# Kernel tuning notes

Measured on AMD Instinct MI355X. Metric: run time of the kernel, lower is better.

The kernel has to match this reference:

```python
import jax, jax.numpy as jnp
import numpy as np

BETA = 0.25
CODEBOOK_SIZE = 8192
EMB_DIM = 256


def setup_inputs() -> dict:
    key = jax.random.key(0)
    k1, k2 = jax.random.split(key)
    z_e = jax.random.normal(k1, (32, 32, 32, EMB_DIM), dtype=jnp.float32)
    codebook = jax.random.normal(k2, (CODEBOOK_SIZE, EMB_DIM), dtype=jnp.float32) * 0.05
    return {"z_e": z_e, "codebook": codebook}


def reference(z_e, codebook):
    sg = jax.lax.stop_gradient
    D = codebook.shape[1]
    z = z_e.reshape(-1, D)                                   # [N, D]
    # squared euclidean distances via ||z||^2 + ||e||^2 - 2 z.e
    z_sq = jnp.sum(z * z, axis=1, keepdims=True)             # [N, 1]
    e_sq = jnp.sum(codebook * codebook, axis=1)              # [K]
    distances = z_sq + e_sq[None, :] - 2.0 * (z @ codebook.T)  # [N, K]
    indices = jnp.argmin(distances, axis=1)                  # [N]
    z_q = codebook[indices].reshape(z_e.shape)               # gather

    commitment = jnp.mean((sg(z_e) - z_q) ** 2)
    codebook_loss = jnp.mean((z_e - sg(z_q)) ** 2)
    z_q_st = z_e + sg(z_q - z_e)
    loss_vq = codebook_loss + BETA * commitment

    # perplexity of assignment distribution (no grad)
    N = z.shape[0]
    counts = jnp.zeros((codebook.shape[0],), jnp.float32).at[indices].add(1.0)
    avg_probs = counts / N
    perplexity = jnp.exp(-jnp.sum(avg_probs * jnp.log(avg_probs + 1e-12)))

    return z_q_st, indices.reshape(z_e.shape[:-1]), loss_vq, perplexity
```

## Files before the change

kernel.cpp:

```cpp
#include <hip/hip_runtime.h>
#include <math.h>

#define N_TOT 32768
#define K_CB 8192
#define D_DIM 256

#define OUT_IDX  (N_TOT * D_DIM)
#define OUT_LOSS (OUT_IDX + N_TOT)
#define OUT_PERP (OUT_LOSS + 1)

#define WS_AIMG   0u
#define AIMG_SZ   (256u * 16u * 8192u)
#define WS_BIMG   (WS_AIMG + AIMG_SZ)
#define BIMG_SZ   (64u * 16u * 8192u)
#define WS_PART   (WS_BIMG + BIMG_SZ)
#define PART_SZ   (16u * 32768u * 16u)
#define WS_ESQ    (WS_PART + PART_SZ)
#define WS_COUNTS (WS_ESQ + 32768u)
#define WS_LPART  (WS_COUNTS + 32768u)

typedef short bf16x8 __attribute__((ext_vector_type(8)));
typedef float f32x4  __attribute__((ext_vector_type(4)));
typedef unsigned short u16x8 __attribute__((ext_vector_type(8)));

__device__ __forceinline__ unsigned short f2bf(float x) {
  unsigned int b = __float_as_uint(x);
  b = b + 0x7FFFu + ((b >> 16) & 1u);
  return (unsigned short)(b >> 16);
}
__device__ __forceinline__ float bf2f(unsigned short h) {
  return __uint_as_float(((unsigned int)h) << 16);
}
__device__ __forceinline__ void gld16(const void* g, void* l) {
  __builtin_amdgcn_global_load_lds(
      (const __attribute__((address_space(1))) void*)g,
      (__attribute__((address_space(3))) void*)l, 16, 0, 0);
}

__global__ __launch_bounds__(256) void prep_z(const float* __restrict__ Z,
                                              char* __restrict__ Aimg) {
  const int tid = threadIdx.x;
  const int row = blockIdx.x * 8 + (tid >> 5);
  const int ch = tid & 31;
  const int kt = ch >> 2, c = ch & 3;
  const int rb = row >> 7, r = row & 127;
  const float4 z0 = *(const float4*)(Z + (size_t)row * D_DIM + kt * 32 + c * 8);
  const float4 z1 = *(const float4*)(Z + (size_t)row * D_DIM + kt * 32 + c * 8 + 4);
  u16x8 h, l;
  h[0] = f2bf(z0.x); l[0] = f2bf(z0.x - bf2f(h[0]));
  h[1] = f2bf(z0.y); l[1] = f2bf(z0.y - bf2f(h[1]));
  h[2] = f2bf(z0.z); l[2] = f2bf(z0.z - bf2f(h[2]));
  h[3] = f2bf(z0.w); l[3] = f2bf(z0.w - bf2f(h[3]));
  h[4] = f2bf(z1.x); l[4] = f2bf(z1.x - bf2f(h[4]));
  h[5] = f2bf(z1.y); l[5] = f2bf(z1.y - bf2f(h[5]));
  h[6] = f2bf(z1.z); l[6] = f2bf(z1.z - bf2f(h[6]));
  h[7] = f2bf(z1.w); l[7] = f2bf(z1.w - bf2f(h[7]));
  const int cs = c ^ ((r >> 1) & 3);
  const size_t off = (size_t)r * 64 + cs * 16;
  *(u16x8*)(Aimg + (size_t)(rb * 16 + kt) * 8192 + off) = h;
  *(u16x8*)(Aimg + (size_t)(rb * 16 + 8 + kt) * 8192 + off) = l;
}

__global__ __launch_bounds__(256) void prep_e(const float* __restrict__ E,
                                              char* __restrict__ Bimg,
                                              float* __restrict__ esqg) {
  const int tid = threadIdx.x;
  const int code = blockIdx.x * 8 + (tid >> 5);
  const int ch = tid & 31;
  const int kt = ch >> 2, c = ch & 3;
  const int ntg = code >> 7, r = code & 127;
  const float4 e0 = *(const float4*)(E + (size_t)code * D_DIM + kt * 32 + c * 8);
  const float4 e1 = *(const float4*)(E + (size_t)code * D_DIM + kt * 32 + c * 8 + 4);
  u16x8 h, l;
  h[0] = f2bf(e0.x); l[0] = f2bf(e0.x - bf2f(h[0]));
  h[1] = f2bf(e0.y); l[1] = f2bf(e0.y - bf2f(h[1]));
  h[2] = f2bf(e0.z); l[2] = f2bf(e0.z - bf2f(h[2]));
  h[3] = f2bf(e0.w); l[3] = f2bf(e0.w - bf2f(h[3]));
  h[4] = f2bf(e1.x); l[4] = f2bf(e1.x - bf2f(h[4]));
  h[5] = f2bf(e1.y); l[5] = f2bf(e1.y - bf2f(h[5]));
  h[6] = f2bf(e1.z); l[6] = f2bf(e1.z - bf2f(h[6]));
  h[7] = f2bf(e1.w); l[7] = f2bf(e1.w - bf2f(h[7]));
  const int cs = c ^ ((r >> 1) & 3);
  const size_t off = (size_t)r * 64 + cs * 16;
  *(u16x8*)(Bimg + (size_t)(ntg * 16 + kt) * 8192 + off) = h;
  *(u16x8*)(Bimg + (size_t)(ntg * 16 + 8 + kt) * 8192 + off) = l;
  float s = e0.x * e0.x + e0.y * e0.y + e0.z * e0.z + e0.w * e0.w +
            e1.x * e1.x + e1.y * e1.y + e1.z * e1.z + e1.w * e1.w;
#pragma unroll
  for (int o = 16; o > 0; o >>= 1) s += __shfl_down(s, o, 32);
  if ((tid & 31) == 0) esqg[code] = s;
}

__global__ __launch_bounds__(256, 2) void argmin_mfma(
    const char* __restrict__ Aimg, const char* __restrict__ Bimg,
    const float* __restrict__ esqg, float4* __restrict__ partials) {
  __shared__ __align__(16) union {
    struct { char Ah[8192]; char Al[8192]; char Bh[8192]; char Bl[8192]; } t[2];
    float4 mbuf[128][2];
  } u;
  __shared__ float esq_s[512];

  const int tid = threadIdx.x;
  const int lane = tid & 63;
  const int wid = tid >> 6;
  const int wrow = wid >> 1, wcol = wid & 1;
  const int lrow = lane & 15, lgrp = lane >> 4;
  const int cb = blockIdx.x & 7;
  const int ntp = (blockIdx.x >> 3) & 1;
  const int rb = blockIdx.x >> 4;
  const int ntg0 = cb * 8 + ntp * 4;

  const int sw = (lrow >> 1) & 3;
  const int aoff = (wrow * 64 + lrow) * 64 + (lgrp ^ sw) * 16;
  const int boff = (wcol * 64 + lrow) * 64 + (lgrp ^ sw) * 16;
  const char* Abase = Aimg + (size_t)rb * (16u * 8192u);
  const char* Bbase0 = Bimg + (size_t)ntg0 * (16u * 8192u);
  const int soff = tid * 16;

  float s1[16], s2[16]; int c1[16], c2[16];
#pragma unroll
  for (int i = 0; i < 16; i++) { s1[i] = 3.4e38f; s2[i] = 3.4e38f; c1[i] = 0; c2[i] = 0; }

#define STAGE_K(kk, BI) do {                                                   \
    const int k_ = (kk) & 7, nti_ = (kk) >> 3;                                 \
    const char* ah_ = Abase + (size_t)k_ * 8192;                               \
    const char* al_ = Abase + (size_t)(8 + k_) * 8192;                         \
    const char* bb_ = Bbase0 + (size_t)nti_ * (16u * 8192u);                   \
    const char* bh_ = bb_ + (size_t)k_ * 8192;                                 \
    const char* bl_ = bb_ + (size_t)(8 + k_) * 8192;                           \
    gld16(ah_ + soff,        u.t[BI].Ah + soff);                               \
    gld16(ah_ + 4096 + soff, u.t[BI].Ah + 4096 + soff);                        \
    gld16(al_ + soff,        u.t[BI].Al + soff);                               \
    gld16(al_ + 4096 + soff, u.t[BI].Al + 4096 + soff);                        \
    gld16(bh_ + soff,        u.t[BI].Bh + soff);                               \
    gld16(bh_ + 4096 + soff, u.t[BI].Bh + 4096 + soff);                        \
    gld16(bl_ + soff,        u.t[BI].Bl + soff);                               \
    gld16(bl_ + 4096 + soff, u.t[BI].Bl + 4096 + soff);                        \
  } while (0)

#define COMPUTE_K(BI) do {                                                     \
    bf16x8 afh[4], afl[4], bfh[4], bfl[4];                                     \
    _Pragma("unroll")                                                          \
    for (int rf = 0; rf < 4; rf++) {                                           \
      afh[rf] = *(const bf16x8*)(u.t[BI].Ah + aoff + rf * 1024);               \
      afl[rf] = *(const bf16x8*)(u.t[BI].Al + aoff + rf * 1024);               \
    }                                                                          \
    _Pragma("unroll")                                                          \
    for (int cf = 0; cf < 4; cf++) {                                           \
      bfh[cf] = *(const bf16x8*)(u.t[BI].Bh + boff + cf * 1024);               \
      bfl[cf] = *(const bf16x8*)(u.t[BI].Bl + boff + cf * 1024);               \
    }                                                                          \
    _Pragma("unroll")                                                          \
    for (int rf = 0; rf < 4; rf++)                                             \
      _Pragma("unroll")                                                        \
      for (int cf = 0; cf < 4; cf++) {                                         \
        acc[rf][cf] = __builtin_amdgcn_mfma_f32_16x16x32_bf16(afh[rf], bfh[cf], acc[rf][cf], 0, 0, 0); \
        acc[rf][cf] = __builtin_amdgcn_mfma_f32_16x16x32_bf16(afh[rf], bfl[cf], acc[rf][cf], 0, 0, 0); \
        acc[rf][cf] = __builtin_amdgcn_mfma_f32_16x16x32_bf16(afl[rf], bfh[cf], acc[rf][cf], 0, 0, 0); \
      }                                                                        \
  } while (0)

  esq_s[tid] = esqg[ntg0 * 128 + tid];
  esq_s[tid + 256] = esqg[ntg0 * 128 + tid + 256];
  STAGE_K(0, 0);

  f32x4 acc[4][4];
#pragma unroll
  for (int i = 0; i < 4; i++)
#pragma unroll
    for (int j = 0; j < 4; j++) acc[i][j] = (f32x4){0.f, 0.f, 0.f, 0.f};

  __syncthreads();

  for (int kp = 0; kp < 16; kp++) {
    const int kk0 = kp * 2;
    STAGE_K(kk0 + 1, 1);
    COMPUTE_K(0);
    __syncthreads();
    if (kp < 15) STAGE_K(kk0 + 2, 0);
    COMPUTE_K(1);
    if ((kp & 3) == 3) {
      const int nti = kp >> 2;
      const int ntg = ntg0 + nti;
      const int code0 = ntg * 128 + wcol * 64 + lrow;
      float eq[4];
#pragma unroll
      for (int cf = 0; cf < 4; cf++) eq[cf] = esq_s[nti * 128 + wcol * 64 + cf * 16 + lrow];
#pragma unroll
      for (int rf = 0; rf < 4; rf++)
#pragma unroll
        for (int reg = 0; reg < 4; reg++) {
          const int r = rf * 4 + reg;
          float v0 = fmaf(-2.f, acc[rf][0][reg], eq[0]);
          float v1 = fmaf(-2.f, acc[rf][1][reg], eq[1]);
          float v2 = fmaf(-2.f, acc[rf][2][reg], eq[2]);
          float v3 = fmaf(-2.f, acc[rf][3][reg], eq[3]);
          float a1 = v0, a2 = v1; int ka1 = code0, ka2 = code0 + 16;
          if (v1 < v0) { a1 = v1; ka1 = code0 + 16; a2 = v0; ka2 = code0; }
          float b1v = v2, b2v = v3; int kb1 = code0 + 32, kb2 = code0 + 48;
          if (v3 < v2) { b1v = v3; kb1 = code0 + 48; b2v = v2; kb2 = code0 + 32; }
          float m1, m2; int k1, k2;
          if (a1 <= b1v) {
            m1 = a1; k1 = ka1;
            if (b1v < a2) { m2 = b1v; k2 = kb1; } else { m2 = a2; k2 = ka2; }
          } else {
            m1 = b1v; k1 = kb1;
            if (a1 <= b2v) { m2 = a1; k2 = ka1; } else { m2 = b2v; k2 = kb2; }
          }
          if (m1 < s1[r]) {
            s2[r] = (m2 < s1[r]) ? m2 : s1[r];
            c2[r] = (m2 < s1[r]) ? k2 : c1[r];
            s1[r] = m1; c1[r] = k1;
          } else if (m1 < s2[r]) {
            s2[r] = m1; c2[r] = k1;
          }
        }
#pragma unroll
      for (int i = 0; i < 4; i++)
#pragma unroll
        for (int j = 0; j < 4; j++) acc[i][j] = (f32x4){0.f, 0.f, 0.f, 0.f};
    }
    __syncthreads();
  }
#undef STAGE_K
#undef COMPUTE_K

#pragma unroll
  for (int r = 0; r < 16; r++) {
#pragma unroll
    for (int m = 1; m <= 8; m <<= 1) {
      float o1 = __shfl_xor(s1[r], m); int k1 = __shfl_xor(c1[r], m);
      float o2 = __shfl_xor(s2[r], m); int k2 = __shfl_xor(c2[r], m);
      bool t1 = (o1 < s1[r]) || (o1 == s1[r] && k1 < c1[r]);
      bool t2 = (o1 < s2[r]) || (o1 == s2[r] && k1 < c2[r]);
      float ns2 = t1 ? s1[r] : (t2 ? o1 : s2[r]);
      int   nc2 = t1 ? c1[r] : (t2 ? k1 : c2[r]);
      s1[r] = t1 ? o1 : s1[r]; c1[r] = t1 ? k1 : c1[r];
      s2[r] = ns2; c2[r] = nc2;
      bool u1 = (o2 < s1[r]) || (o2 == s1[r] && k2 < c1[r]);
      bool u2 = (o2 < s2[r]) || (o2 == s2[r] && k2 < c2[r]);
      ns2 = u1 ? s1[r] : (u2 ? o2 : s2[r]);
      nc2 = u1 ? c1[r] : (u2 ? k2 : c2[r]);
      s1[r] = u1 ? o2 : s1[r]; c1[r] = u1 ? k2 : c1[r];
      s2[r] = ns2; c2[r] = nc2;
    }
  }

  __syncthreads();
  if (lrow == 0) {
#pragma unroll
    for (int rf = 0; rf < 4; rf++)
#pragma unroll
      for (int reg = 0; reg < 4; reg++) {
        const int r = rf * 4 + reg;
        const int row = wrow * 64 + rf * 16 + lgrp * 4 + reg;
        float4 p;
        p.x = s1[r]; p.y = __int_as_float(c1[r]);
        p.z = s2[r]; p.w = __int_as_float(c2[r]);
        u.mbuf[row][wcol] = p;
      }
  }
  __syncthreads();
  if (tid < 128) {
    float4 pa = u.mbuf[tid][0];
    float4 pb = u.mbuf[tid][1];
    float D1 = pa.x; int C1 = __float_as_int(pa.y);
    float D2 = pa.z; int C2 = __float_as_int(pa.w);
    float a = pb.x; int ka = __float_as_int(pb.y);
    float b = pb.z; int kb = __float_as_int(pb.w);
    if (a < D1 || (a == D1 && ka < C1)) { D2 = D1; C2 = C1; D1 = a; C1 = ka; }
    else if (a < D2 || (a == D2 && ka < C2)) { D2 = a; C2 = ka; }
    if (b < D1 || (b == D1 && kb < C1)) { D2 = D1; C2 = C1; D1 = b; C1 = kb; }
    else if (b < D2 || (b == D2 && kb < C2)) { D2 = b; C2 = kb; }
    float4 p;
    p.x = D1; p.y = __int_as_float(C1); p.z = D2; p.w = __int_as_float(C2);
    partials[(size_t)(ntp * 8 + cb) * N_TOT + rb * 128 + tid] = p;
  }
}

__global__ __launch_bounds__(128) void merge_rescore(
    const float* __restrict__ Z, const float* __restrict__ E,
    const float4* __restrict__ partials, float* __restrict__ out_idx_f) {
  const int row = blockIdx.x * 128 + threadIdx.x;
  float D1 = 3.4e38f, D2 = 3.4e38f; int C1 = 0, C2 = 0;
  for (int s = 0; s < 16; s++) {
    float4 p = partials[(size_t)s * N_TOT + row];
    float a = p.x; int ka = __float_as_int(p.y);
    float b = p.z; int kb = __float_as_int(p.w);
    if (a < D1 || (a == D1 && ka < C1)) { D2 = D1; C2 = C1; D1 = a; C1 = ka; }
    else if (a < D2 || (a == D2 && ka < C2)) { D2 = a; C2 = ka; }
    if (b < D1 || (b == D1 && kb < C1)) { D2 = D1; C2 = C1; D1 = b; C1 = kb; }
    else if (b < D2 || (b == D2 && kb < C2)) { D2 = b; C2 = kb; }
  }
  const float* zp = Z + (size_t)row * D_DIM;
  const float* ep1 = E + (size_t)C1 * D_DIM;
  const float* ep2 = E + (size_t)C2 * D_DIM;
  double dd1 = 0.0, dd2 = 0.0;
  for (int d = 0; d < D_DIM; d += 4) {
    const float4 zv = *(const float4*)(zp + d);
    const float4 e1v = *(const float4*)(ep1 + d);
    const float4 e2v = *(const float4*)(ep2 + d);
    double t;
    t = (double)zv.x - (double)e1v.x; dd1 += t * t;
    t = (double)zv.y - (double)e1v.y; dd1 += t * t;
    t = (double)zv.z - (double)e1v.z; dd1 += t * t;
    t = (double)zv.w - (double)e1v.w; dd1 += t * t;
    t = (double)zv.x - (double)e2v.x; dd2 += t * t;
    t = (double)zv.y - (double)e2v.y; dd2 += t * t;
    t = (double)zv.z - (double)e2v.z; dd2 += t * t;
    t = (double)zv.w - (double)e2v.w; dd2 += t * t;
  }
  int fin = C1;
  if (dd2 < dd1 || (dd2 == dd1 && C2 < C1)) fin = C2;
  out_idx_f[row] = (float)fin;
}

__global__ __launch_bounds__(256) void gather_kernel(
    const float* __restrict__ Z, const float* __restrict__ E,
    const float* __restrict__ idx_f, float* __restrict__ zq_out,
    float* __restrict__ counts, float* __restrict__ loss_part) {
  const int t = threadIdx.x;
  float lsum = 0.0f;
  for (int rr = 0; rr < 16; rr++) {
    const int row = blockIdx.x * 16 + rr;
    const int c = (int)idx_f[row];
    const float e = E[(size_t)c * D_DIM + t];
    const float z = Z[(size_t)row * D_DIM + t];
    zq_out[(size_t)row * D_DIM + t] = e;
    const float d = z - e;
    lsum += d * d;
    if (t == 0) atomicAdd(&counts[c], 1.0f);
  }
#pragma unroll
  for (int off = 32; off > 0; off >>= 1) lsum += __shfl_down(lsum, off);
  __shared__ float wsum[4];
  if ((t & 63) == 0) wsum[t >> 6] = lsum;
  __syncthreads();
  if (t == 0) loss_part[blockIdx.x] = wsum[0] + wsum[1] + wsum[2] + wsum[3];
}

__global__ __launch_bounds__(256) void final_kernel(
    const float* __restrict__ counts, const float* __restrict__ loss_part,
    float* __restrict__ out) {
  const int t = threadIdx.x;
  float h = 0.0f, ls = 0.0f;
  for (int k = t; k < K_CB; k += 256) {
    const float p = counts[k] * (1.0f / (float)N_TOT);
    h += p * logf(p + 1e-12f);
  }
  for (int k = t; k < 2048; k += 256) ls += loss_part[k];
#pragma unroll
  for (int off = 32; off > 0; off >>= 1) {
    h += __shfl_down(h, off);
    ls += __shfl_down(ls, off);
  }
  __shared__ float ws4[4], ls4[4];
  if ((t & 63) == 0) { ws4[t >> 6] = h; ls4[t >> 6] = ls; }
  __syncthreads();
  if (t == 0) {
    const float H = ws4[0] + ws4[1] + ws4[2] + ws4[3];
    const float L = ls4[0] + ls4[1] + ls4[2] + ls4[3];
    out[OUT_LOSS] = 1.25f * L * (1.0f / (float)(N_TOT * D_DIM));
    out[OUT_PERP] = expf(-H);
  }
}

extern "C" void kernel_launch(void* const* d_in, const int* in_sizes, int n_in,
                              void* d_out, int out_size, void* d_ws, size_t ws_size,
                              hipStream_t stream) {
  (void)in_sizes; (void)n_in; (void)out_size; (void)ws_size;
  const float* Z = (const float*)d_in[0];
  const float* E = (const float*)d_in[1];
  float* out = (float*)d_out;
  char* ws = (char*)d_ws;
  char* Aimg = ws + WS_AIMG;
  char* Bimg = ws + WS_BIMG;
  float4* partials = (float4*)(ws + WS_PART);
  float* esqg = (float*)(ws + WS_ESQ);
  float* counts = (float*)(ws + WS_COUNTS);
  float* loss_part = (float*)(ws + WS_LPART);

  hipMemsetAsync(ws + WS_COUNTS, 0, 32768, stream);
  prep_z<<<dim3(4096), dim3(256), 0, stream>>>(Z, Aimg);
  prep_e<<<dim3(1024), dim3(256), 0, stream>>>(E, Bimg, esqg);
  argmin_mfma<<<dim3(4096), dim3(256), 0, stream>>>(Aimg, Bimg, esqg, partials);
  merge_rescore<<<dim3(256), dim3(128), 0, stream>>>(Z, E, partials, out + OUT_IDX);
  gather_kernel<<<dim3(2048), dim3(256), 0, stream>>>(Z, E, out + OUT_IDX, out, counts, loss_part);
  final_kernel<<<dim3(1), dim3(256), 0, stream>>>(counts, loss_part, out);
}
```

Baseline: 666.8 us.

## Enlarge argmin MFMA tile to 256x256 with 8 waves and s_setprio scheduling

The distance GEMM kernel moves from 128x128 tiles with 4 waves to 256x256 tiles with 8 waves per block, 512 codes per block and half as many blocks. This raises arithmetic intensity and cuts redundant global loads of the A and B images. The main loop now uses explicit barriers with vmcnt waits and s_setprio around the MFMA groups to overlap staging with compute. Running top-2 state moves from registers into an LDS merge buffer per epilogue. The change doubles LDS use to about 128KB and doubles accumulator registers, which risks lower occupancy or spills.

```diff
diff --git a/kernel.cpp b/kernel.cpp
--- a/kernel.cpp
+++ b/kernel.cpp
@@ -91,190 +91,199 @@
   if ((tid & 31) == 0) esqg[code] = s;
 }
 
-__global__ __launch_bounds__(256, 2) void argmin_mfma(
+__global__ __launch_bounds__(512, 2) void argmin_mfma(
     const char* __restrict__ Aimg, const char* __restrict__ Bimg,
     const float* __restrict__ esqg, float4* __restrict__ partials) {
-  __shared__ __align__(16) union {
-    struct { char Ah[8192]; char Al[8192]; char Bh[8192]; char Bl[8192]; } t[2];
-    float4 mbuf[128][2];
-  } u;
+  __shared__ __align__(16) struct { char Ah[16384]; char Al[16384];
+                                    char Bh[16384]; char Bl[16384]; } lds[2];
+  __shared__ __align__(16) float4 mrg[256][4];
   __shared__ float esq_s[512];
 
   const int tid = threadIdx.x;
   const int lane = tid & 63;
   const int wid = tid >> 6;
-  const int wrow = wid >> 1, wcol = wid & 1;
+  const int wrow = wid >> 2, wcol = wid & 3;
   const int lrow = lane & 15, lgrp = lane >> 4;
-  const int cb = blockIdx.x & 7;
-  const int ntp = (blockIdx.x >> 3) & 1;
   const int rb = blockIdx.x >> 4;
-  const int ntg0 = cb * 8 + ntp * 4;
+  const int ct = blockIdx.x & 15;
+  const int rb2 = rb * 2;
+  const int so = tid * 16;
 
   const int sw = (lrow >> 1) & 3;
-  const int aoff = (wrow * 64 + lrow) * 64 + (lgrp ^ sw) * 16;
-  const int boff = (wcol * 64 + lrow) * 64 + (lgrp ^ sw) * 16;
-  const char* Abase = Aimg + (size_t)rb * (16u * 8192u);
-  const char* Bbase0 = Bimg + (size_t)ntg0 * (16u * 8192u);
-  const int soff = tid * 16;
-
-  float s1[16], s2[16]; int c1[16], c2[16];
-#pragma unroll
-  for (int i = 0; i < 16; i++) { s1[i] = 3.4e38f; s2[i] = 3.4e38f; c1[i] = 0; c2[i] = 0; }
-
-#define STAGE_K(kk, BI) do {                                                   \
-    const int k_ = (kk) & 7, nti_ = (kk) >> 3;                                 \
-    const char* ah_ = Abase + (size_t)k_ * 8192;                               \
-    const char* al_ = Abase + (size_t)(8 + k_) * 8192;                         \
-    const char* bb_ = Bbase0 + (size_t)nti_ * (16u * 8192u);                   \
-    const char* bh_ = bb_ + (size_t)k_ * 8192;                                 \
-    const char* bl_ = bb_ + (size_t)(8 + k_) * 8192;                           \
-    gld16(ah_ + soff,        u.t[BI].Ah + soff);                               \
-    gld16(ah_ + 4096 + soff, u.t[BI].Ah + 4096 + soff);                        \
-    gld16(al_ + soff,        u.t[BI].Al + soff);                               \
-    gld16(al_ + 4096 + soff, u.t[BI].Al + 4096 + soff);                        \
-    gld16(bh_ + soff,        u.t[BI].Bh + soff);                               \
-    gld16(bh_ + 4096 + soff, u.t[BI].Bh + 4096 + soff);                        \
-    gld16(bl_ + soff,        u.t[BI].Bl + soff);                               \
-    gld16(bl_ + 4096 + soff, u.t[BI].Bl + 4096 + soff);                        \
+  const int slot = (lgrp ^ sw) * 16;
+  const int abase = wrow * 8192 + lrow * 64 + slot;
+  const int bbase = (wcol >> 1) * 8192 + ((wcol & 1) * 64 + lrow) * 64 + slot;
+
+#define STAGE_K(cn, BI) do {                                                   \
+    const int k_ = (cn) & 7, t_ = (cn) >> 3;                                   \
+    const int ga_ = rb2 * 16 + k_, gb_ = (rb2 + 1) * 16 + k_;                  \
+    const int g0_ = (ct * 4 + t_ * 2) * 16 + k_, g1_ = g0_ + 16;               \
+    gld16(Aimg + (size_t)ga_ * 8192 + so,       lds[BI].Ah + so);              \
+    gld16(Aimg + (size_t)gb_ * 8192 + so,       lds[BI].Ah + 8192 + so);       \
+    gld16(Aimg + (size_t)(ga_ + 8) * 8192 + so, lds[BI].Al + so);              \
+    gld16(Aimg + (size_t)(gb_ + 8) * 8192 + so, lds[BI].Al + 8192 + so);       \
+    gld16(Bimg + (size_t)g0_ * 8192 + so,       lds[BI].Bh + so);              \
+    gld16(Bimg + (size_t)g1_ * 8192 + so,       lds[BI].Bh + 8192 + so);       \
+    gld16(Bimg + (size_t)(g0_ + 8) * 8192 + so, lds[BI].Bl + so);              \
+    gld16(Bimg + (size_t)(g1_ + 8) * 8192 + so, lds[BI].Bl + 8192 + so);       \
   } while (0)
 
 #define COMPUTE_K(BI) do {                                                     \
-    bf16x8 afh[4], afl[4], bfh[4], bfl[4];                                     \
-    _Pragma("unroll")                                                          \
-    for (int rf = 0; rf < 4; rf++) {                                           \
-      afh[rf] = *(const bf16x8*)(u.t[BI].Ah + aoff + rf * 1024);               \
-      afl[rf] = *(const bf16x8*)(u.t[BI].Al + aoff + rf * 1024);               \
+    bf16x8 fa[8], fb[4], fc[4];                                                \
+    _Pragma("unroll")                                                          \
+    for (int rf = 0; rf < 8; rf++)                                             \
+      fa[rf] = *(const bf16x8*)(lds[BI].Ah + abase + rf * 1024);               \
+    _Pragma("unroll")                                                          \
+    for (int cf = 0; cf < 4; cf++)                                             \
+      fb[cf] = *(const bf16x8*)(lds[BI].Bh + bbase + cf * 1024);               \
+    __builtin_amdgcn_s_setprio(1);                                             \
+    _Pragma("unroll")                                                          \
+    for (int rf = 0; rf < 8; rf++)                                             \
+      _Pragma("unroll")                                                        \
+      for (int cf = 0; cf < 4; cf++)                                           \
+        acc[rf][cf] = __builtin_amdgcn_mfma_f32_16x16x32_bf16(fa[rf], fb[cf], acc[rf][cf], 0, 0, 0); \
+    __builtin_amdgcn_s_setprio(0);                                             \
+    _Pragma("unroll")                                                          \
+    for (int cf = 0; cf < 4; cf++)                                             \
+      fc[cf] = *(const bf16x8*)(lds[BI].Bl + bbase + cf * 1024);               \
+    __builtin_amdgcn_s_setprio(1);                                             \
+    _Pragma("unroll")                                                          \
+    for (int rf = 0; rf < 8; rf++)                                             \
+      _Pragma("unroll")                                                        \
+      for (int cf = 0; cf < 4; cf++)                                           \
+        acc[rf][cf] = __builtin_amdgcn_mfma_f32_16x16x32_bf16(fa[rf], fc[cf], acc[rf][cf], 0, 0, 0); \
+    __builtin_amdgcn_s_setprio(0);                                             \
+    _Pragma("unroll")                                                          \
+    for (int rf = 0; rf < 8; rf++)                                             \
+      fa[rf] = *(const bf16x8*)(lds[BI].Al + abase + rf * 1024);               \
+    __builtin_amdgcn_s_setprio(1);                                             \
+    _Pragma("unroll")                                                          \
+    for (int rf = 0; rf < 8; rf++)                                             \
+      _Pragma("unroll")                                                        \
+      for (int cf = 0; cf < 4; cf++)                                           \
+        acc[rf][cf] = __builtin_amdgcn_mfma_f32_16x16x32_bf16(fa[rf], fb[cf], acc[rf][cf], 0, 0, 0); \
+    __builtin_amdgcn_s_setprio(0);                                             \
+  } while (0)
+
+#define CHUNK(c_, BI, DOSTAGE) do {                                            \
+    __builtin_amdgcn_sched_barrier(0);                                         \
+    __builtin_amdgcn_s_barrier();                                              \
+    if (DOSTAGE) { STAGE_K((c_) + 1, (BI) ^ 1);                                \
+                   asm volatile("s_waitcnt vmcnt(8)" ::: "memory"); }          \
+    else         { asm volatile("s_waitcnt vmcnt(0)" ::: "memory"); }          \
+    __builtin_amdgcn_s_barrier();                                              \
+    __builtin_amdgcn_sched_barrier(0);                                         \
+    COMPUTE_K(BI);                                                             \
+  } while (0)
+
+#define EPILOGUE(T) do {                                                       \
+    const float eqA = esq_s[(T) * 256 + wcol * 64 + lrow];                     \
+    const float eqB = esq_s[(T) * 256 + wcol * 64 + 16 + lrow];                \
+    const float eqC = esq_s[(T) * 256 + wcol * 64 + 32 + lrow];                \
+    const float eqD = esq_s[(T) * 256 + wcol * 64 + 48 + lrow];                \
+    const int code0 = ct * 512 + (T) * 256 + wcol * 64 + lrow;                 \
+    _Pragma("unroll")                                                          \
+    for (int rf = 0; rf < 8; rf++)                                             \
+      _Pragma("unroll")                                                        \
+      for (int reg = 0; reg < 4; reg++) {                                      \
+        float v0 = fmaf(-2.f, acc[rf][0][reg], eqA);                           \
+        float v1 = fmaf(-2.f, acc[rf][1][reg], eqB);                           \
+        float v2 = fmaf(-2.f, acc[rf][2][reg], eqC);                           \
+        float v3 = fmaf(-2.f, acc[rf][3][reg], eqD);                           \
+        float a1 = v0, a2 = v1; int ka1 = code0, ka2 = code0 + 16;             \
+        if (v1 < v0) { a1 = v1; ka1 = code0 + 16; a2 = v0; ka2 = code0; }      \
+        float b1 = v2, b2 = v3; int kb1 = code0 + 32, kb2 = code0 + 48;        \
+        if (v3 < v2) { b1 = v3; kb1 = code0 + 48; b2 = v2; kb2 = code0 + 32; } \
+        float m1, m2; int k1, k2;                                              \
+        if (a1 <= b1) { m1 = a1; k1 = ka1;                                     \
+          if (b1 < a2) { m2 = b1; k2 = kb1; } else { m2 = a2; k2 = ka2; } }    \
+        else { m1 = b1; k1 = kb1;                                              \
+          if (a1 <= b2) { m2 = a1; k2 = ka1; } else { m2 = b2; k2 = kb2; } }   \
+        _Pragma("unroll")                                                      \
+        for (int mm = 1; mm <= 8; mm <<= 1) {                                  \
+          float o1 = __shfl_xor(m1, mm); int j1 = __shfl_xor(k1, mm);          \
+          float o2 = __shfl_xor(m2, mm); int j2 = __shfl_xor(k2, mm);          \
+          bool t1 = (o1 < m1) || (o1 == m1 && j1 < k1);                        \
+          bool t2 = (o1 < m2) || (o1 == m2 && j1 < k2);                        \
+          float ns2 = t1 ? m1 : (t2 ? o1 : m2);                                \
+          int   nc2 = t1 ? k1 : (t2 ? j1 : k2);                                \
+          m1 = t1 ? o1 : m1; k1 = t1 ? j1 : k1; m2 = ns2; k2 = nc2;            \
+          bool u1 = (o2 < m1) || (o2 == m1 && j2 < k1);                        \
+          bool u2 = (o2 < m2) || (o2 == m2 && j2 < k2);                        \
+          ns2 = u1 ? m1 : (u2 ? o2 : m2);                                      \
+          nc2 = u1 ? k1 : (u2 ? j2 : k2);                                      \
+          m1 = u1 ? o2 : m1; k1 = u1 ? j2 : k1; m2 = ns2; k2 = nc2;            \
+        }                                                                      \
+        if (lrow == 0) {                                                       \
+          const int row = wrow * 128 + rf * 16 + lgrp * 4 + reg;               \
+          if ((T) == 0) {                                                      \
+            float4 p; p.x = m1; p.y = __int_as_float(k1);                      \
+            p.z = m2; p.w = __int_as_float(k2);                                \
+            mrg[row][wcol] = p;                                                \
+          } else {                                                             \
+            float4 p = mrg[row][wcol];                                         \
+            float D1 = p.x; int C1 = __float_as_int(p.y);                      \
+            float D2 = p.z; int C2 = __float_as_int(p.w);                      \
+            if (m1 < D1 || (m1 == D1 && k1 < C1)) { D2 = D1; C2 = C1; D1 = m1; C1 = k1; } \
+            else if (m1 < D2 || (m1 == D2 && k1 < C2)) { D2 = m1; C2 = k1; }   \
+            if (m2 < D1 || (m2 == D1 && k2 < C1)) { D2 = D1; C2 = C1; D1 = m2; C1 = k2; } \
+            else if (m2 < D2 || (m2 == D2 && k2 < C2)) { D2 = m2; C2 = k2; }   \
+            p.x = D1; p.y = __int_as_float(C1);                                \
+            p.z = D2; p.w = __int_as_float(C2);                                \
+            mrg[row][wcol] = p;                                                \
+          }                                                                    \
+        }                                                                      \
+      }                                                                        \
+    if ((T) == 0) {                                                            \
+      _Pragma("unroll")                                                        \
+      for (int i = 0; i < 8; i++)                                              \
+        _Pragma("unroll")                                                      \
+        for (int j = 0; j < 4; j++) acc[i][j] = (f32x4){0.f, 0.f, 0.f, 0.f};   \
     }                                                                          \
-    _Pragma("unroll")                                                          \
-    for (int cf = 0; cf < 4; cf++) {                                           \
-      bfh[cf] = *(const bf16x8*)(u.t[BI].Bh + boff + cf * 1024);               \
-      bfl[cf] = *(const bf16x8*)(u.t[BI].Bl + boff + cf * 1024);               \
-    }                                                                          \
-    _Pragma("unroll")                                                          \
-    for (int rf = 0; rf < 4; rf++)                                             \
-      _Pragma("unroll")                                                        \
-      for (int cf = 0; cf < 4; cf++) {                                         \
-        acc[rf][cf] = __builtin_amdgcn_mfma_f32_16x16x32_bf16(afh[rf], bfh[cf], acc[rf][cf], 0, 0, 0); \
-        acc[rf][cf] = __builtin_amdgcn_mfma_f32_16x16x32_bf16(afh[rf], bfl[cf], acc[rf][cf], 0, 0, 0); \
-        acc[rf][cf] = __builtin_amdgcn_mfma_f32_16x16x32_bf16(afl[rf], bfh[cf], acc[rf][cf], 0, 0, 0); \
-      }                                                                        \
   } while (0)
 
-  esq_s[tid] = esqg[ntg0 * 128 + tid];
-  esq_s[tid + 256] = esqg[ntg0 * 128 + tid + 256];
+  f32x4 acc[8][4];
+#pragma unroll
+  for (int i = 0; i < 8; i++)
+#pragma unroll
+    for (int j = 0; j < 4; j++) acc[i][j] = (f32x4){0.f, 0.f, 0.f, 0.f};
+
+  esq_s[tid] = esqg[ct * 512 + tid];
   STAGE_K(0, 0);
-
-  f32x4 acc[4][4];
-#pragma unroll
-  for (int i = 0; i < 4; i++)
-#pragma unroll
-    for (int j = 0; j < 4; j++) acc[i][j] = (f32x4){0.f, 0.f, 0.f, 0.f};
-
   __syncthreads();
 
-  for (int kp = 0; kp < 16; kp++) {
-    const int kk0 = kp * 2;
-    STAGE_K(kk0 + 1, 1);
-    COMPUTE_K(0);
-    __syncthreads();
-    if (kp < 15) STAGE_K(kk0 + 2, 0);
-    COMPUTE_K(1);
-    if ((kp & 3) == 3) {
-      const int nti = kp >> 2;
-      const int ntg = ntg0 + nti;
-      const int code0 = ntg * 128 + wcol * 64 + lrow;
-      float eq[4];
-#pragma unroll
-      for (int cf = 0; cf < 4; cf++) eq[cf] = esq_s[nti * 128 + wcol * 64 + cf * 16 + lrow];
-#pragma unroll
-      for (int rf = 0; rf < 4; rf++)
-#pragma unroll
-        for (int reg = 0; reg < 4; reg++) {
-          const int r = rf * 4 + reg;
-          float v0 = fmaf(-2.f, acc[rf][0][reg], eq[0]);
-          float v1 = fmaf(-2.f, acc[rf][1][reg], eq[1]);
-          float v2 = fmaf(-2.f, acc[rf][2][reg], eq[2]);
-          float v3 = fmaf(-2.f, acc[rf][3][reg], eq[3]);
-          float a1 = v0, a2 = v1; int ka1 = code0, ka2 = code0 + 16;
-          if (v1 < v0) { a1 = v1; ka1 = code0 + 16; a2 = v0; ka2 = code0; }
-          float b1v = v2, b2v = v3; int kb1 = code0 + 32, kb2 = code0 + 48;
-          if (v3 < v2) { b1v = v3; kb1 = code0 + 48; b2v = v2; kb2 = code0 + 32; }
-          float m1, m2; int k1, k2;
-          if (a1 <= b1v) {
-            m1 = a1; k1 = ka1;
-            if (b1v < a2) { m2 = b1v; k2 = kb1; } else { m2 = a2; k2 = ka2; }
-          } else {
-            m1 = b1v; k1 = kb1;
-            if (a1 <= b2v) { m2 = a1; k2 = ka1; } else { m2 = b2v; k2 = kb2; }
-          }
-          if (m1 < s1[r]) {
-            s2[r] = (m2 < s1[r]) ? m2 : s1[r];
-            c2[r] = (m2 < s1[r]) ? k2 : c1[r];
-            s1[r] = m1; c1[r] = k1;
-          } else if (m1 < s2[r]) {
-            s2[r] = m1; c2[r] = k1;
-          }
-        }
-#pragma unroll
-      for (int i = 0; i < 4; i++)
-#pragma unroll
-        for (int j = 0; j < 4; j++) acc[i][j] = (f32x4){0.f, 0.f, 0.f, 0.f};
-    }
-    __syncthreads();
-  }
+  for (int c2 = 0; c2 < 8; c2++) {
+    const int c0 = c2 * 2;
+    CHUNK(c0, 0, 1);
+    if (c2 < 7) CHUNK(c0 + 1, 1, 1);
+    else        CHUNK(15, 1, 0);
+    if (c2 == 3) EPILOGUE(0);
+  }
+  EPILOGUE(1);
+
 #undef STAGE_K
 #undef COMPUTE_K
-
-#pragma unroll
-  for (int r = 0; r < 16; r++) {
-#pragma unroll
-    for (int m = 1; m <= 8; m <<= 1) {
-      float o1 = __shfl_xor(s1[r], m); int k1 = __shfl_xor(c1[r], m);
-      float o2 = __shfl_xor(s2[r], m); int k2 = __shfl_xor(c2[r], m);
-      bool t1 = (o1 < s1[r]) || (o1 == s1[r] && k1 < c1[r]);
-      bool t2 = (o1 < s2[r]) || (o1 == s2[r] && k1 < c2[r]);
-      float ns2 = t1 ? s1[r] : (t2 ? o1 : s2[r]);
-      int   nc2 = t1 ? c1[r] : (t2 ? k1 : c2[r]);
-      s1[r] = t1 ? o1 : s1[r]; c1[r] = t1 ? k1 : c1[r];
-      s2[r] = ns2; c2[r] = nc2;
-      bool u1 = (o2 < s1[r]) || (o2 == s1[r] && k2 < c1[r]);
-      bool u2 = (o2 < s2[r]) || (o2 == s2[r] && k2 < c2[r]);
-      ns2 = u1 ? s1[r] : (u2 ? o2 : s2[r]);
-      nc2 = u1 ? c1[r] : (u2 ? k2 : c2[r]);
-      s1[r] = u1 ? o2 : s1[r]; c1[r] = u1 ? k2 : c1[r];
-      s2[r] = ns2; c2[r] = nc2;
+#undef CHUNK
+#undef EPILOGUE
+
+  __syncthreads();
+  if (tid < 256) {
+    float4 q = mrg[tid][0];
+    float D1 = q.x; int C1 = __float_as_int(q.y);
+    float D2 = q.z; int C2 = __float_as_int(q.w);
+#pragma unroll
+    for (int w = 1; w < 4; w++) {
+      float4 p = mrg[tid][w];
+      float a = p.x; int ka = __float_as_int(p.y);
+      float b = p.z; int kb = __float_as_int(p.w);
+      if (a < D1 || (a == D1 && ka < C1)) { D2 = D1; C2 = C1; D1 = a; C1 = ka; }
+      else if (a < D2 || (a == D2 && ka < C2)) { D2 = a; C2 = ka; }
+      if (b < D1 || (b == D1 && kb < C1)) { D2 = D1; C2 = C1; D1 = b; C1 = kb; }
+      else if (b < D2 || (b == D2 && kb < C2)) { D2 = b; C2 = kb; }
     }
-  }
-
-  __syncthreads();
-  if (lrow == 0) {
-#pragma unroll
-    for (int rf = 0; rf < 4; rf++)
-#pragma unroll
-      for (int reg = 0; reg < 4; reg++) {
-        const int r = rf * 4 + reg;
-        const int row = wrow * 64 + rf * 16 + lgrp * 4 + reg;
-        float4 p;
-        p.x = s1[r]; p.y = __int_as_float(c1[r]);
-        p.z = s2[r]; p.w = __int_as_float(c2[r]);
-        u.mbuf[row][wcol] = p;
-      }
-  }
-  __syncthreads();
-  if (tid < 128) {
-    float4 pa = u.mbuf[tid][0];
-    float4 pb = u.mbuf[tid][1];
-    float D1 = pa.x; int C1 = __float_as_int(pa.y);
-    float D2 = pa.z; int C2 = __float_as_int(pa.w);
-    float a = pb.x; int ka = __float_as_int(pb.y);
-    float b = pb.z; int kb = __float_as_int(pb.w);
-    if (a < D1 || (a == D1 && ka < C1)) { D2 = D1; C2 = C1; D1 = a; C1 = ka; }
-    else if (a < D2 || (a == D2 && ka < C2)) { D2 = a; C2 = ka; }
-    if (b < D1 || (b == D1 && kb < C1)) { D2 = D1; C2 = C1; D1 = b; C1 = kb; }
-    else if (b < D2 || (b == D2 && kb < C2)) { D2 = b; C2 = kb; }
     float4 p;
     p.x = D1; p.y = __int_as_float(C1); p.z = D2; p.w = __int_as_float(C2);
-    partials[(size_t)(ntp * 8 + cb) * N_TOT + rb * 128 + tid] = p;
+    partials[(size_t)ct * N_TOT + rb * 256 + tid] = p;
   }
 }
 
@@ -383,7 +392,7 @@
   hipMemsetAsync(ws + WS_COUNTS, 0, 32768, stream);
   prep_z<<<dim3(4096), dim3(256), 0, stream>>>(Z, Aimg);
   prep_e<<<dim3(1024), dim3(256), 0, stream>>>(E, Bimg, esqg);
-  argmin_mfma<<<dim3(4096), dim3(256), 0, stream>>>(Aimg, Bimg, esqg, partials);
+  argmin_mfma<<<dim3(2048), dim3(512), 0, stream>>>(Aimg, Bimg, esqg, partials);
   merge_rescore<<<dim3(256), dim3(128), 0, stream>>>(Z, E, partials, out + OUT_IDX);
   gather_kernel<<<dim3(2048), dim3(256), 0, stream>>>(Z, E, out + OUT_IDX, out, counts, loss_part);
   final_kernel<<<dim3(1), dim3(256), 0, stream>>>(counts, loss_part, out);
```

After: 1.876 ms. 2.81x slower.

## Restructure GEMM main loop with explicit vmcnt waits, barriers and MFMA priority

Applied to the files above, without the earlier changes.

Replaces the two-stage-per-iteration loop with a fully unrolled 32-step loop that issues the next K-slice's async global-to-LDS loads and then waits only on the older loads via an explicit s_waitcnt vmcnt(8), surrounded by raw s_barrier and sched_barrier fences. The MFMA block is split into three phases (hi*hi, hi*lo, lo*hi), each wrapped in s_setprio to favour the matrix work, and the argmin epilogue is moved into a macro called every 8 steps. The goal is to overlap loads with MFMA and cut synchronisation stalls. The cost is hand-tuned wait counts that depend on how many loads STAGE_K issues, plus larger code from full unrolling.

```diff
diff --git a/kernel.cpp b/kernel.cpp
--- a/kernel.cpp
+++ b/kernel.cpp
@@ -150,14 +150,65 @@
       bfh[cf] = *(const bf16x8*)(u.t[BI].Bh + boff + cf * 1024);               \
       bfl[cf] = *(const bf16x8*)(u.t[BI].Bl + boff + cf * 1024);               \
     }                                                                          \
+    __builtin_amdgcn_s_setprio(1);                                             \
     _Pragma("unroll")                                                          \
     for (int rf = 0; rf < 4; rf++)                                             \
       _Pragma("unroll")                                                        \
-      for (int cf = 0; cf < 4; cf++) {                                         \
+      for (int cf = 0; cf < 4; cf++)                                           \
         acc[rf][cf] = __builtin_amdgcn_mfma_f32_16x16x32_bf16(afh[rf], bfh[cf], acc[rf][cf], 0, 0, 0); \
+    __builtin_amdgcn_s_setprio(0);                                             \
+    __builtin_amdgcn_s_setprio(1);                                             \
+    _Pragma("unroll")                                                          \
+    for (int rf = 0; rf < 4; rf++)                                             \
+      _Pragma("unroll")                                                        \
+      for (int cf = 0; cf < 4; cf++)                                           \
         acc[rf][cf] = __builtin_amdgcn_mfma_f32_16x16x32_bf16(afh[rf], bfl[cf], acc[rf][cf], 0, 0, 0); \
+    __builtin_amdgcn_s_setprio(0);                                             \
+    __builtin_amdgcn_s_setprio(1);                                             \
+    _Pragma("unroll")                                                          \
+    for (int rf = 0; rf < 4; rf++)                                             \
+      _Pragma("unroll")                                                        \
+      for (int cf = 0; cf < 4; cf++)                                           \
         acc[rf][cf] = __builtin_amdgcn_mfma_f32_16x16x32_bf16(afl[rf], bfh[cf], acc[rf][cf], 0, 0, 0); \
+    __builtin_amdgcn_s_setprio(0);                                             \
+  } while (0)
+
+#define EPILOGUE(T) do {                                                       \
+    const int code0 = (ntg0 + (T)) * 128 + wcol * 64 + lrow;                   \
+    float eq0 = esq_s[(T) * 128 + wcol * 64 + lrow];                           \
+    float eq1 = esq_s[(T) * 128 + wcol * 64 + 16 + lrow];                      \
+    float eq2 = esq_s[(T) * 128 + wcol * 64 + 32 + lrow];                      \
+    float eq3 = esq_s[(T) * 128 + wcol * 64 + 48 + lrow];                      \
+    _Pragma("unroll")                                                          \
+    for (int rf = 0; rf < 4; rf++)                                             \
+      _Pragma("unroll")                                                        \
+      for (int reg = 0; reg < 4; reg++) {                                      \
+        const int r = rf * 4 + reg;                                            \
+        float v0 = fmaf(-2.f, acc[rf][0][reg], eq0);                           \
+        float v1 = fmaf(-2.f, acc[rf][1][reg], eq1);                           \
+        float v2 = fmaf(-2.f, acc[rf][2][reg], eq2);                           \
+        float v3 = fmaf(-2.f, acc[rf][3][reg], eq3);                           \
+        float a1 = v0, a2 = v1; int ka1 = code0, ka2 = code0 + 16;             \
+        if (v1 < v0) { a1 = v1; ka1 = code0 + 16; a2 = v0; ka2 = code0; }      \
+        float b1v = v2, b2v = v3; int kb1 = code0 + 32, kb2 = code0 + 48;      \
+        if (v3 < v2) { b1v = v3; kb1 = code0 + 48; b2v = v2; kb2 = code0 + 32; } \
+        float m1, m2; int k1, k2;                                              \
+        if (a1 <= b1v) { m1 = a1; k1 = ka1;                                    \
+          if (b1v < a2) { m2 = b1v; k2 = kb1; } else { m2 = a2; k2 = ka2; } }  \
+        else { m1 = b1v; k1 = kb1;                                             \
+          if (a1 <= b2v) { m2 = a1; k2 = ka1; } else { m2 = b2v; k2 = kb2; } } \
+        if (m1 < s1[r]) {                                                      \
+          s2[r] = (m2 < s1[r]) ? m2 : s1[r];                                   \
+          c2[r] = (m2 < s1[r]) ? k2 : c1[r];                                   \
+          s1[r] = m1; c1[r] = k1;                                              \
+        } else if (m1 < s2[r]) {                                               \
+          s2[r] = m1; c2[r] = k1;                                              \
+        }                                                                      \
       }                                                                        \
+    _Pragma("unroll")                                                          \
+    for (int i = 0; i < 4; i++)                                                \
+      _Pragma("unroll")                                                        \
+      for (int j = 0; j < 4; j++) acc[i][j] = (f32x4){0.f, 0.f, 0.f, 0.f};     \
   } while (0)
 
   esq_s[tid] = esqg[ntg0 * 128 + tid];
@@ -172,58 +223,25 @@
 
   __syncthreads();
 
-  for (int kp = 0; kp < 16; kp++) {
-    const int kk0 = kp * 2;
-    STAGE_K(kk0 + 1, 1);
-    COMPUTE_K(0);
-    __syncthreads();
-    if (kp < 15) STAGE_K(kk0 + 2, 0);
-    COMPUTE_K(1);
-    if ((kp & 3) == 3) {
-      const int nti = kp >> 2;
-      const int ntg = ntg0 + nti;
-      const int code0 = ntg * 128 + wcol * 64 + lrow;
-      float eq[4];
-#pragma unroll
-      for (int cf = 0; cf < 4; cf++) eq[cf] = esq_s[nti * 128 + wcol * 64 + cf * 16 + lrow];
-#pragma unroll
-      for (int rf = 0; rf < 4; rf++)
-#pragma unroll
-        for (int reg = 0; reg < 4; reg++) {
-          const int r = rf * 4 + reg;
-          float v0 = fmaf(-2.f, acc[rf][0][reg], eq[0]);
-          float v1 = fmaf(-2.f, acc[rf][1][reg], eq[1]);
-          float v2 = fmaf(-2.f, acc[rf][2][reg], eq[2]);
-          float v3 = fmaf(-2.f, acc[rf][3][reg], eq[3]);
-          float a1 = v0, a2 = v1; int ka1 = code0, ka2 = code0 + 16;
-          if (v1 < v0) { a1 = v1; ka1 = code0 + 16; a2 = v0; ka2 = code0; }
-          float b1v = v2, b2v = v3; int kb1 = code0 + 32, kb2 = code0 + 48;
-          if (v3 < v2) { b1v = v3; kb1 = code0 + 48; b2v = v2; kb2 = code0 + 32; }
-          float m1, m2; int k1, k2;
-          if (a1 <= b1v) {
-            m1 = a1; k1 = ka1;
-            if (b1v < a2) { m2 = b1v; k2 = kb1; } else { m2 = a2; k2 = ka2; }
-          } else {
-            m1 = b1v; k1 = kb1;
-            if (a1 <= b2v) { m2 = a1; k2 = ka1; } else { m2 = b2v; k2 = kb2; }
-          }
-          if (m1 < s1[r]) {
-            s2[r] = (m2 < s1[r]) ? m2 : s1[r];
-            c2[r] = (m2 < s1[r]) ? k2 : c1[r];
-            s1[r] = m1; c1[r] = k1;
-          } else if (m1 < s2[r]) {
-            s2[r] = m1; c2[r] = k1;
-          }
-        }
-#pragma unroll
-      for (int i = 0; i < 4; i++)
-#pragma unroll
-        for (int j = 0; j < 4; j++) acc[i][j] = (f32x4){0.f, 0.f, 0.f, 0.f};
+#pragma unroll
+  for (int c = 0; c < 32; c++) {
+    const int bi = c & 1;
+    __builtin_amdgcn_sched_barrier(0);
+    __builtin_amdgcn_s_barrier();
+    if (c < 31) {
+      STAGE_K(c + 1, bi ^ 1);
+      asm volatile("s_waitcnt vmcnt(8)" ::: "memory");
+    } else {
+      asm volatile("s_waitcnt vmcnt(0)" ::: "memory");
     }
-    __syncthreads();
+    __builtin_amdgcn_s_barrier();
+    __builtin_amdgcn_sched_barrier(0);
+    COMPUTE_K(bi);
+    if ((c & 7) == 7) EPILOGUE(c >> 3);
   }
 #undef STAGE_K
 #undef COMPUTE_K
+#undef EPILOGUE
 
 #pragma unroll
   for (int r = 0; r < 16; r++) {
```

After: 665.3 us. Within noise of the previous version (-0.2%).
